# Performance work log

Measured on AMD Instinct MI355X. Metric: run time of the kernel, lower is better.

Reference implementation:

```python
import jax, jax.numpy as jnp
import numpy as np

B, H, W = 8, 512, 512
N_INST = 8
N_SIGMA = 2
FG_W = 1.0
W_INST, W_VAR, W_SEED = 1.0, 10.0, 1.0


def make_yxm():
    xm = jnp.broadcast_to(jnp.linspace(0.0, 1.0, W)[None, None, :], (1, H, W))
    ym = jnp.broadcast_to(jnp.linspace(0.0, 1.0, H)[None, :, None], (1, H, W))
    return jnp.concatenate([ym, xm], 0)  # [2,H,W]


def lovasz_hinge(logits, labels):
    # logits, labels: [P]; labels in {0,1}
    signs = 2.0 * labels - 1.0
    errors = 1.0 - logits * signs
    order = jnp.argsort(-errors)
    errors_s = errors[order]
    gt_s = labels[order]
    gts = gt_s.sum()
    intersection = gts - jnp.cumsum(gt_s)
    union = gts + jnp.cumsum(1.0 - gt_s)
    jac = 1.0 - intersection / union
    jac = jnp.concatenate([jac[:1], jac[1:] - jac[:-1]])
    return jnp.dot(jax.nn.relu(errors_s), jax.lax.stop_gradient(jac))


def seg_item(pred, inst, label, center_img, yxm):
    spatial_emb = jnp.tanh(pred[0:2]) + yxm            # [2,H,W]
    sigma = jax.nn.sigmoid(pred[2:2 + N_SIGMA])        # [2,H,W]
    seed = jax.nn.sigmoid(pred[2 + N_SIGMA])           # [H,W]
    seed_loss = jnp.sum(jnp.where(label == 0, seed * seed, 0.0))

    def per_inst(iid):
        in_mask = (inst == iid)
        cmask = in_mask & center_img
        valid = (cmask.sum() == 1)                      # exactly one center pixel
        m = in_mask.astype(pred.dtype)
        npix = jnp.maximum(m.sum(), 1.0)
        center = jnp.sum(yxm * cmask, axis=(1, 2))      # [2]
        s_mean = jnp.sum(sigma * m, axis=(1, 2)) / npix # [2]
        var_l = jnp.sum(((sigma - jax.lax.stop_gradient(s_mean)[:, None, None]) ** 2) * m) / (N_SIGMA * npix)
        s = jnp.exp(s_mean * 10.0)
        dist = jnp.exp(-jnp.sum(((spatial_emb - center[:, None, None]) ** 2) * s[:, None, None], axis=0))
        inst_l = lovasz_hinge((dist * 2.0 - 1.0).ravel(), m.ravel())
        seed_l = jnp.sum(((seed - jax.lax.stop_gradient(dist)) ** 2) * m)
        v = valid.astype(pred.dtype)
        return inst_l * v, var_l * v, seed_l * v

    il, vl, sl = jax.vmap(per_inst)(jnp.arange(1, N_INST + 1))
    # NOTE: source never increments obj_count in the seg loop, so no division.
    seed_total = (seed_loss + FG_W * sl.sum()) / (H * W)
    return W_INST * il.sum() + W_VAR * vl.sum() + W_SEED * seed_total


def tra_item(pred, inst, center_img, offset, yxm):
    emb = yxm - jnp.tanh(pred[0:2])
    sigma = jax.nn.sigmoid(pred[2:2 + N_SIGMA])

    def per_inst(iid):
        in_mask = (inst == iid)
        cmask = in_mask & center_img
        center = jnp.sum(yxm * cmask, axis=(1, 2))          # [2]
        off_c = jnp.sum(offset * cmask, axis=(1, 2))        # [2]
        gt_c = center - off_c / 256.0
        valid = (cmask.sum() == 1) & (gt_c.min() >= 0.0) & (gt_c.max() <= 1.0)
        m = in_mask.astype(pred.dtype)
        npix = jnp.maximum(m.sum(), 1.0)
        s_mean = jnp.sum(sigma * m, axis=(1, 2)) / npix
        var_l = jnp.sum(((sigma - jax.lax.stop_gradient(s_mean)[:, None, None]) ** 2) * m)  # sum (not mean)
        s = jnp.exp(s_mean * 10.0)
        dist = jnp.exp(-jnp.sum(((emb - gt_c[:, None, None]) ** 2) * s[:, None, None], axis=0))
        tl = lovasz_hinge((dist * 2.0 - 1.0).ravel(), m.ravel())
        v = valid.astype(pred.dtype)
        return tl * v, var_l * v, v

    tl, vl, vs = jax.vmap(per_inst)(jnp.arange(1, N_INST + 1))
    cnt = jnp.maximum(vs.sum(), 1.0)
    return W_INST * (tl.sum() / cnt) + W_VAR * (vl.sum() / cnt)


def setup_inputs() -> dict:
    key = jax.random.key(0)
    k1, k2, k3 = jax.random.split(key, 3)
    inst = np.zeros((H, W), np.int32)
    cen = np.zeros((H, W), bool)
    for i in range(N_INST):
        ty, tx = i // 2, i % 2
        cy, cx = ty * 128 + 64, tx * 256 + 128
        inst[cy - 40:cy + 40, cx - 40:cx + 40] = i + 1
        cen[cy, cx] = True
    instances = jnp.tile(jnp.asarray(inst)[None], (B, 1, 1))
    center_images = jnp.tile(jnp.asarray(cen)[None], (B, 1, 1))
    labels = (instances > 0).astype(jnp.int32)
    return {
        "segmentation_predictions": jax.random.normal(k1, (B, 3 + N_SIGMA, H, W), jnp.float32),
        "tracking_predictions": jax.random.normal(k2, (B // 2, 2 + N_SIGMA, H, W), jnp.float32),
        "instances": instances,
        "labels": labels,
        "center_images": center_images,
        "offsets": jax.random.normal(k3, (B // 2, 2, H, W), jnp.float32),
    }


def reference(segmentation_predictions, tracking_predictions, instances, labels, center_images, offsets):
    yxm = make_yxm()
    seg = jax.vmap(seg_item, in_axes=(0, 0, 0, 0, None))(
        segmentation_predictions, instances, labels, center_images, yxm)
    half = B // 2
    tra = jax.vmap(tra_item, in_axes=(0, 0, 0, 0, None))(
        tracking_predictions, instances[:half], center_images[:half], offsets, yxm)
    return seg.sum() + tra.sum()
```

## Files before the change

### kernel.cpp

```cpp
#include <hip/hip_runtime.h>
#include <cstdint>
#include <cstddef>

#define HW (512 * 512)
#define NB 128
#define NPAIR 96
#define THRQ 4.9f
#define BSCALE 64.0f

#define W_HNEG 0
#define W_HPOS (NPAIR * NB)
#define W_SEEDL (NPAIR * NB * 2)
#define W_CNT (W_SEEDL + NPAIR)
#define NZERO (W_CNT + 1)
#define W_PART 24704
#define W_POUT (W_PART + 12 * 82 * 64)

__device__ __forceinline__ float sigmoidf_(float x) {
    return 1.0f / (1.0f + __expf(-x));
}
__device__ __forceinline__ float tanhf_(float x) {
    float e = __expf(2.0f * x);
    return 1.0f - 2.0f / (e + 1.0f);
}
__device__ __forceinline__ float wred(float v) {
#pragma unroll
    for (int o = 32; o > 0; o >>= 1) v += __shfl_down(v, o, 64);
    return v;
}
__device__ __forceinline__ unsigned wredu(unsigned v) {
#pragma unroll
    for (int o = 32; o > 0; o >>= 1) v += __shfl_down(v, o, 64);
    return v;
}

__global__ __launch_bounds__(256) void reduce_nc(
    const float* __restrict__ segp, const float* __restrict__ trap,
    const int* __restrict__ inst, const int* __restrict__ cen,
    const float* __restrict__ off, float* __restrict__ ws)
{
    __shared__ float wavepart[4][41];
    __shared__ float centacc[40];
    int item = blockIdx.y;
    bool isseg = item < 8;
    int ii = isseg ? item : item - 8;
    int bx = blockIdx.x, tid = threadIdx.x;

    {
        int w = (item * 64 + bx) * 33 + tid;
        if (tid < 33 && w < NZERO) ws[w] = 0.0f;
    }
    if (tid < 40) centacc[tid] = 0.0f;
    __syncthreads();

    const float* pb = isseg ? segp + (size_t)item * 5 * HW
                            : trap + (size_t)ii * 4 * HW;
    const int* ib = inst + (size_t)ii * HW;
    const int* cb = cen + (size_t)ii * HW;
    const float* ob = off + (size_t)ii * 2 * HW;

    float npx[8], a0[8], q0[8], a1[8], q1[8];
#pragma unroll
    for (int j = 0; j < 8; j++) { npx[j]=0.f; a0[j]=0.f; q0[j]=0.f; a1[j]=0.f; q1[j]=0.f; }
    float sacc = 0.f;

    int base = bx * 4096;
    for (int it = 0; it < 4; ++it) {
        int idx = base + (it * 256 + tid) * 4;
        int4 v4 = *(const int4*)&ib[idx];
        const int vs[4] = { v4.x, v4.y, v4.z, v4.w };
        if (isseg) {
            float4 x4 = *(const float4*)&pb[4 * HW + idx];
            const float ss[4] = { x4.x, x4.y, x4.z, x4.w };
#pragma unroll
            for (int c = 0; c < 4; c++) {
                if (vs[c] == 0) { float sd = sigmoidf_(ss[c]); sacc += sd * sd; }
            }
        }
        if ((v4.x | v4.y | v4.z | v4.w) != 0) {
            float4 x2 = *(const float4*)&pb[2 * HW + idx];
            float4 x3 = *(const float4*)&pb[3 * HW + idx];
            int4 c4 = *(const int4*)&cb[idx];
            const float s2s[4] = { x2.x, x2.y, x2.z, x2.w };
            const float s3s[4] = { x3.x, x3.y, x3.z, x3.w };
            const int cs[4] = { c4.x, c4.y, c4.z, c4.w };
#pragma unroll
            for (int c = 0; c < 4; c++) {
                int v = vs[c];
                if (v == 0) continue;
                float s0 = sigmoidf_(s2s[c]);
                float s1 = sigmoidf_(s3s[c]);
                float s00 = s0 * s0, s11 = s1 * s1;
#pragma unroll
                for (int j = 0; j < 8; j++) {
                    float f = (v == j + 1) ? 1.0f : 0.0f;
                    npx[j] += f;
                    a0[j] += f * s0; q0[j] += f * s00;
                    a1[j] += f * s1; q1[j] += f * s11;
                }
                if (cs[c] != 0 && v >= 1 && v <= 8) {
                    int idxc = idx + c;
                    int cb5 = (v - 1) * 5;
                    int y = idxc >> 9, x = idxc & 511;
                    atomicAdd(&centacc[cb5 + 0], (float)y * (1.0f / 511.0f));
                    atomicAdd(&centacc[cb5 + 1], (float)x * (1.0f / 511.0f));
                    atomicAdd(&centacc[cb5 + 2], 1.0f);
                    if (!isseg) {
                        atomicAdd(&centacc[cb5 + 3], ob[idxc]);
                        atomicAdd(&centacc[cb5 + 4], ob[HW + idxc]);
                    }
                }
            }
        }
    }
    int lane = tid & 63, wave = tid >> 6;
#pragma unroll
    for (int j = 0; j < 8; j++) {
        float r0 = wred(npx[j]), r1 = wred(a0[j]), r2 = wred(q0[j]);
        float r3 = wred(a1[j]), r4 = wred(q1[j]);
        if (lane == 0) {
            wavepart[wave][j * 5 + 0] = r0; wavepart[wave][j * 5 + 1] = r1;
            wavepart[wave][j * 5 + 2] = r2; wavepart[wave][j * 5 + 3] = r3;
            wavepart[wave][j * 5 + 4] = r4;
        }
    }
    {
        float rs = wred(sacc);
        if (lane == 0) wavepart[wave][40] = rs;
    }
    __syncthreads();
    float* pit = ws + W_PART + item * 82 * 64;
    if (tid < 40) {
        pit[tid * 64 + bx] = wavepart[0][tid] + wavepart[1][tid] + wavepart[2][tid] + wavepart[3][tid];
    } else if (tid == 40) {
        pit[80 * 64 + bx] = wavepart[0][40] + wavepart[1][40] + wavepart[2][40] + wavepart[3][40];
    } else if (tid >= 41 && tid < 81) {
        pit[(40 + tid - 41) * 64 + bx] = centacc[tid - 41];
    } else if (tid == 81) {
        pit[81 * 64 + bx] = 0.0f;
    }
}

__global__ __launch_bounds__(256) void hist_k(
    const float* __restrict__ segp, const float* __restrict__ trap,
    const int* __restrict__ inst, const float* __restrict__ ws,
    unsigned* __restrict__ hneg, unsigned* __restrict__ hpos,
    float* __restrict__ seedl)
{
    __shared__ unsigned hh[8 * NB + 8];
    __shared__ float csum[82];
    __shared__ float prm[8][4];
    int item = blockIdx.y;
    bool isseg = item < 8;
    int ii = isseg ? item : item - 8;
    int tid = threadIdx.x;
    int pairBase = (isseg ? 0 : 64) + ii * 8;

    for (int i = tid; i < 8 * NB + 8; i += 256) hh[i] = 0u;
    if (tid < 82) {
        const float* pit = ws + W_PART + item * 82 * 64 + tid * 64;
        float s = 0.f;
#pragma unroll 8
        for (int b = 0; b < 64; b++) s += pit[b];
        csum[tid] = s;
    }
    __syncthreads();
    if (tid < 8) {
        int j = tid;
        float np = fmaxf(csum[j * 5], 1.0f);
        float cy = csum[40 + j * 5], cx = csum[40 + j * 5 + 1];
        if (!isseg) {
            cy -= csum[40 + j * 5 + 3] * (1.0f / 256.0f);
            cx -= csum[40 + j * 5 + 4] * (1.0f / 256.0f);
        }
        prm[j][0] = cy;
        prm[j][1] = cx;
        prm[j][2] = __expf(10.0f * csum[j * 5 + 1] / np);
        prm[j][3] = __expf(10.0f * csum[j * 5 + 3] / np);
    }
    __syncthreads();

    float cyR[8], cxR[8], s0R[8], s1R[8];
#pragma unroll
    for (int j = 0; j < 8; j++) {
        cyR[j] = prm[j][0]; cxR[j] = prm[j][1];
        s0R[j] = prm[j][2]; s1R[j] = prm[j][3];
    }
    const float* pb = isseg ? segp + (size_t)item * 5 * HW
                            : trap + (size_t)ii * 4 * HW;
    const int* ib = inst + (size_t)ii * HW;

    unsigned cnt0[8];
#pragma unroll
    for (int j = 0; j < 8; j++) cnt0[j] = 0u;

    int base = blockIdx.x * 4096;
    for (int it = 0; it < 4; ++it) {
        int idx = base + (it * 256 + tid) * 4;
        int4 v4 = *(const int4*)&ib[idx];
        float4 f0 = *(const float4*)&pb[idx];
        float4 f1 = *(const float4*)&pb[HW + idx];
        const int vv[4] = { v4.x, v4.y, v4.z, v4.w };
        const float p0s[4] = { f0.x, f0.y, f0.z, f0.w };
        const float p1s[4] = { f1.x, f1.y, f1.z, f1.w };
#pragma unroll
        for (int c = 0; c < 4; c++) {
            int idxc = idx + c;
            int v = vv[c];
            int y = idxc >> 9, x = idxc & 511;
            float ym = (float)y * (1.0f / 511.0f);
            float xm = (float)x * (1.0f / 511.0f);
            float t0 = tanhf_(p0s[c]), t1 = tanhf_(p1s[c]);
            float e0 = isseg ? (t0 + ym) : (ym - t0);
            float e1 = isseg ? (t1 + xm) : (xm - t1);
            unsigned sbits = 0u;
#pragma unroll
            for (int j = 0; j < 8; j++) {
                float d0 = e0 - cyR[j], d1 = e1 - cxR[j];
                float q = fmaf(d0 * d0, s0R[j], d1 * d1 * s1R[j]);
                bool m = (v == j + 1);
                bool slow = m || (q <= THRQ);
                sbits |= (slow ? 1u : 0u) << j;
                cnt0[j] += slow ? 0u : 1u;
            }
            while (sbits) {
                int j = __ffs(sbits) - 1;
                sbits &= sbits - 1u;
                float d0 = e0 - prm[j][0], d1 = e1 - prm[j][1];
                float q = fmaf(d0 * d0, prm[j][2], d1 * d1 * prm[j][3]);
                float dd = __expf(-q);
                bool m = (v == j + 1);
                float e = m ? fmaf(-2.0f, dd, 2.0f) : 2.0f * dd;
                int bin = (int)(e * BSCALE);
                if (bin > NB - 1) bin = NB - 1;
                atomicAdd(&hh[j * NB + bin], m ? 0x10000u : 1u);
                if (m && isseg) {
                    float sd = sigmoidf_(pb[4 * HW + idxc]);
                    float df = sd - dd;
                    atomicAdd((float*)&hh[8 * NB + j], df * df);
                }
            }
        }
    }
    int lane = tid & 63;
#pragma unroll
    for (int j = 0; j < 8; j++) {
        unsigned r = wredu(cnt0[j]);
        if (lane == 0 && r) atomicAdd(&hh[j * NB], r);
    }
    __syncthreads();

#pragma unroll
    for (int j = 0; j < 8; j++) {
        size_t gb = (size_t)(pairBase + j) * NB;
        for (int i = tid & 127; i < NB; i += 128) {
            if ((tid >> 7) == 0 || 1) {}
        }
        for (int i = tid; i < NB; i += 256) {
            unsigned hv = hh[j * NB + i];
            if (hv) {
                unsigned n = hv & 0xFFFFu, p = hv >> 16;
                if (n) atomicAdd(&hneg[gb + i], n);
                if (p) atomicAdd(&hpos[gb + i], p);
            }
        }
    }
    if (isseg && tid < 8) {
        float sv = __uint_as_float(hh[8 * NB + tid]);
        if (sv != 0.0f) atomicAdd(&seedl[pairBase + tid], sv);
    }
}

__global__ __launch_bounds__(64) void scanfin_k(
    float* __restrict__ ws, const unsigned* __restrict__ hneg,
    const unsigned* __restrict__ hpos, const float* __restrict__ seedl,
    unsigned* __restrict__ cntr, float* __restrict__ out)
{
    __shared__ float fin[NPAIR * 4 + 8];
    int p = blockIdx.x;
    int lane = threadIdx.x;
    int item12 = (p < 64) ? (p >> 3) : (8 + ((p - 64) >> 3));
    int j = p & 7;
    const float* pit = ws + W_PART + item12 * 82 * 64;

    float r0 = pit[(j * 5 + 0) * 64 + lane];
    float r1 = pit[(j * 5 + 1) * 64 + lane];
    float r2 = pit[(j * 5 + 2) * 64 + lane];
    float r3 = pit[(j * 5 + 3) * 64 + lane];
    float r4 = pit[(j * 5 + 4) * 64 + lane];
    float c0 = pit[(40 + j * 5 + 0) * 64 + lane];
    float c1 = pit[(40 + j * 5 + 1) * 64 + lane];
    float c2 = pit[(40 + j * 5 + 2) * 64 + lane];
    float c3 = pit[(40 + j * 5 + 3) * 64 + lane];
    float c4 = pit[(40 + j * 5 + 4) * 64 + lane];
    r0 = wred(r0); r1 = wred(r1); r2 = wred(r2); r3 = wred(r3); r4 = wred(r4);
    c0 = wred(c0); c1 = wred(c1); c2 = wred(c2); c3 = wred(c3); c4 = wred(c4);

    const unsigned* hn = hneg + (size_t)p * NB;
    const unsigned* hp = hpos + (size_t)p * NB;
    unsigned hnv[2], hpv[2];
    float ck = 0.f, cp = 0.f;
#pragma unroll
    for (int i = 0; i < 2; i++) {
        int bn = NB - 1 - (lane * 2 + i);
        unsigned a = hn[bn], b = hp[bn];
        hnv[i] = a; hpv[i] = b;
        ck += (float)(a + b); cp += (float)b;
    }
    float ik = ck, ip = cp;
#pragma unroll
    for (int o = 1; o < 64; o <<= 1) {
        float nk = __shfl_up(ik, o, 64), np2 = __shfl_up(ip, o, 64);
        if (lane >= o) { ik += nk; ip += np2; }
    }
    float P = __shfl(ip, 63, 64);
    float k = ik - ck, pp = ip - cp;
    float acc = 0.f;
#pragma unroll
    for (int i = 0; i < 2; i++) {
        float cn = (float)hnv[i], cpp = (float)hpv[i];
        float c = cn + cpp;
        if (c > 0.f) {
            float Jb = (k > 0.f) ? (1.0f - (P - pp) / (P + k - pp)) : 0.0f;
            k += c; pp += cpp;
            float Ja = 1.0f - (P - pp) / (P + k - pp);
            int bn = NB - 1 - (lane * 2 + i);
            acc += ((float)bn + 0.5f) * (2.0f / NB) * (Ja - Jb);
        }
    }
    acc = wred(acc);

    if (lane == 0) {
        float np = fmaxf(r0, 1.0f);
        float v0 = fmaxf(r2 - r1 * r1 / np, 0.0f);
        float v1 = fmaxf(r4 - r3 * r3 / np, 0.0f);
        float valid, varl;
        if (p < 64) {
            varl = (v0 + v1) / (2.0f * np);
            valid = (c2 > 0.5f && c2 < 1.5f) ? 1.0f : 0.0f;
        } else {
            varl = v0 + v1;
            float gy = c0 - c3 * (1.0f / 256.0f);
            float gx = c1 - c4 * (1.0f / 256.0f);
            valid = (c2 > 0.5f && c2 < 1.5f &&
                     gy >= 0.0f && gy <= 1.0f && gx >= 0.0f && gx <= 1.0f) ? 1.0f : 0.0f;
        }
        float* po = ws + W_POUT + p * 4;
        po[0] = acc; po[1] = valid; po[2] = varl; po[3] = 0.0f;
    }
    __threadfence();
    unsigned old = 0;
    if (lane == 0) old = atomicAdd(cntr, 1u);
    old = (unsigned)__shfl((int)old, 0, 64);
    if (old != NPAIR - 1) return;

    __threadfence();
    volatile float* pv = ws + W_POUT;
    for (int q = lane; q < NPAIR; q += 64) {
        fin[q * 4 + 0] = pv[q * 4 + 0];
        fin[q * 4 + 1] = pv[q * 4 + 1];
        fin[q * 4 + 2] = pv[q * 4 + 2];
        fin[q * 4 + 3] = seedl[q];
    }
#pragma unroll
    for (int b = 0; b < 8; b++) {
        float s = ws[W_PART + b * 82 * 64 + 80 * 64 + lane];
        s = wred(s);
        if (lane == 0) fin[NPAIR * 4 + b] = s;
    }
    __syncthreads();
    if (lane == 0) {
        double total = 0.0;
        for (int b = 0; b < 8; b++) {
            double s = 0.0, sl = 0.0;
            for (int jj = 0; jj < 8; jj++) {
                int pr = b * 8 + jj;
                double v = fin[pr * 4 + 1];
                s += v * ((double)fin[pr * 4 + 0] + 10.0 * (double)fin[pr * 4 + 2]);
                sl += v * (double)fin[pr * 4 + 3];
            }
            total += s + ((double)fin[NPAIR * 4 + b] + sl) / (double)HW;
        }
        for (int tt = 0; tt < 4; tt++) {
            double tl = 0.0, vl = 0.0, cnt = 0.0;
            for (int jj = 0; jj < 8; jj++) {
                int pr = 64 + tt * 8 + jj;
                double v = fin[pr * 4 + 1];
                tl += v * (double)fin[pr * 4 + 0];
                vl += v * (double)fin[pr * 4 + 2];
                cnt += v;
            }
            if (cnt < 1.0) cnt = 1.0;
            total += tl / cnt + 10.0 * vl / cnt;
        }
        *out = (float)total;
    }
}

extern "C" void kernel_launch(void* const* d_in, const int* in_sizes, int n_in,
                              void* d_out, int out_size, void* d_ws, size_t ws_size,
                              hipStream_t stream)
{
    const float* segp = (const float*)d_in[0];
    const float* trap = (const float*)d_in[1];
    const int* inst   = (const int*)d_in[2];
    const int* cen    = (const int*)d_in[4];
    const float* off  = (const float*)d_in[5];
    float* out = (float*)d_out;

    float* ws = (float*)d_ws;
    unsigned* hneg = (unsigned*)d_ws + W_HNEG;
    unsigned* hpos = (unsigned*)d_ws + W_HPOS;
    float* seedl = ws + W_SEEDL;
    unsigned* cntr = (unsigned*)d_ws + W_CNT;

    reduce_nc<<<dim3(64, 12), 256, 0, stream>>>(segp, trap, inst, cen, off, ws);
    hist_k<<<dim3(64, 12), 256, 0, stream>>>(segp, trap, inst, ws, hneg, hpos, seedl);
    scanfin_k<<<NPAIR, 64, 0, stream>>>(ws, hneg, hpos, seedl, cntr, out);
}
```

Before: 64.03 us.

## Add coarse LUT culling of instances, split column-sum kernel, double grid blocks

The reduction and histogram kernels now use 128 blocks per item instead of 64, each covering half as many pixels, to expose more parallelism. A new small kernel reduces the per-block partials once and precomputes per-instance parameters, so the histogram and final kernels no longer repeat that reduction in every block. The histogram kernel builds a shared-memory 48x64 lookup table over embedding space that conservatively marks which instances can fall under the distance threshold. Each pixel then evaluates only those candidates plus its own instance, instead of testing all eight, and the count of far-away pixels is recovered from per-block totals. The cost is an extra launch, per-block LUT construction, and an assumption that embeddings stay inside the LUT's range.

```diff
diff --git a/kernel.cpp b/kernel.cpp
--- a/kernel.cpp
+++ b/kernel.cpp
@@ -7,6 +7,7 @@
 #define NPAIR 96
 #define THRQ 4.9f
 #define BSCALE 64.0f
+#define RB 128
 
 #define W_HNEG 0
 #define W_HPOS (NPAIR * NB)
@@ -14,7 +15,9 @@
 #define W_CNT (W_SEEDL + NPAIR)
 #define NZERO (W_CNT + 1)
 #define W_PART 24704
-#define W_POUT (W_PART + 12 * 82 * 64)
+#define W_CSUM (W_PART + 12 * 81 * RB)
+#define W_PRM (W_CSUM + 12 * 81)
+#define W_POUT (W_PRM + 12 * 32)
 
 __device__ __forceinline__ float sigmoidf_(float x) {
     return 1.0f / (1.0f + __expf(-x));
@@ -28,13 +31,8 @@
     for (int o = 32; o > 0; o >>= 1) v += __shfl_down(v, o, 64);
     return v;
 }
-__device__ __forceinline__ unsigned wredu(unsigned v) {
-#pragma unroll
-    for (int o = 32; o > 0; o >>= 1) v += __shfl_down(v, o, 64);
-    return v;
-}
-
-__global__ __launch_bounds__(256) void reduce_nc(
+
+__global__ __launch_bounds__(256) void reduce_k(
     const float* __restrict__ segp, const float* __restrict__ trap,
     const int* __restrict__ inst, const int* __restrict__ cen,
     const float* __restrict__ off, float* __restrict__ ws)
@@ -47,8 +45,8 @@
     int bx = blockIdx.x, tid = threadIdx.x;
 
     {
-        int w = (item * 64 + bx) * 33 + tid;
-        if (tid < 33 && w < NZERO) ws[w] = 0.0f;
+        int gb = (item * RB + bx) * 17 + tid;
+        if (tid < 17 && gb < NZERO) ws[gb] = 0.0f;
     }
     if (tid < 40) centacc[tid] = 0.0f;
     __syncthreads();
@@ -64,8 +62,9 @@
     for (int j = 0; j < 8; j++) { npx[j]=0.f; a0[j]=0.f; q0[j]=0.f; a1[j]=0.f; q1[j]=0.f; }
     float sacc = 0.f;
 
-    int base = bx * 4096;
-    for (int it = 0; it < 4; ++it) {
+    int base = bx * 2048;
+#pragma unroll
+    for (int it = 0; it < 2; ++it) {
         int idx = base + (it * 256 + tid) * 4;
         int4 v4 = *(const int4*)&ib[idx];
         const int vs[4] = { v4.x, v4.y, v4.z, v4.w };
@@ -78,12 +77,12 @@
             }
         }
         if ((v4.x | v4.y | v4.z | v4.w) != 0) {
+            int4 c4 = *(const int4*)&cb[idx];
             float4 x2 = *(const float4*)&pb[2 * HW + idx];
             float4 x3 = *(const float4*)&pb[3 * HW + idx];
-            int4 c4 = *(const int4*)&cb[idx];
+            const int cs[4] = { c4.x, c4.y, c4.z, c4.w };
             const float s2s[4] = { x2.x, x2.y, x2.z, x2.w };
             const float s3s[4] = { x3.x, x3.y, x3.z, x3.w };
-            const int cs[4] = { c4.x, c4.y, c4.z, c4.w };
 #pragma unroll
             for (int c = 0; c < 4; c++) {
                 int v = vs[c];
@@ -129,73 +128,92 @@
         if (lane == 0) wavepart[wave][40] = rs;
     }
     __syncthreads();
-    float* pit = ws + W_PART + item * 82 * 64;
+    float* pit = ws + W_PART + (size_t)item * 81 * RB;
     if (tid < 40) {
-        pit[tid * 64 + bx] = wavepart[0][tid] + wavepart[1][tid] + wavepart[2][tid] + wavepart[3][tid];
+        pit[tid * RB + bx] = wavepart[0][tid] + wavepart[1][tid] + wavepart[2][tid] + wavepart[3][tid];
     } else if (tid == 40) {
-        pit[80 * 64 + bx] = wavepart[0][40] + wavepart[1][40] + wavepart[2][40] + wavepart[3][40];
-    } else if (tid >= 41 && tid < 81) {
-        pit[(40 + tid - 41) * 64 + bx] = centacc[tid - 41];
-    } else if (tid == 81) {
-        pit[81 * 64 + bx] = 0.0f;
+        pit[80 * RB + bx] = wavepart[0][40] + wavepart[1][40] + wavepart[2][40] + wavepart[3][40];
+    } else if (tid < 81) {
+        pit[(tid - 1) * RB + bx] = centacc[tid - 41];
+    }
+}
+
+__global__ __launch_bounds__(256) void csum_k(float* __restrict__ ws)
+{
+    __shared__ float csh[81];
+    int item = blockIdx.x, tid = threadIdx.x;
+    bool isseg = item < 8;
+    if (tid < 162) {
+        int comp = tid >> 1;
+        const float* p = ws + W_PART + (size_t)item * 81 * RB + comp * RB + (tid & 1) * 64;
+        float s = 0.f;
+#pragma unroll 8
+        for (int i = 0; i < 64; i++) s += p[i];
+        s += __shfl_xor(s, 1, 64);
+        if ((tid & 1) == 0) csh[comp] = s;
+    }
+    __syncthreads();
+    if (tid < 81) ws[W_CSUM + item * 81 + tid] = csh[tid];
+    if (tid < 8) {
+        int j = tid;
+        float np = fmaxf(csh[j * 5], 1.0f);
+        float cy = csh[40 + j * 5], cx = csh[40 + j * 5 + 1];
+        if (!isseg) {
+            cy -= csh[40 + j * 5 + 3] * (1.0f / 256.0f);
+            cx -= csh[40 + j * 5 + 4] * (1.0f / 256.0f);
+        }
+        float* o = ws + W_PRM + item * 32 + j * 4;
+        o[0] = cy;
+        o[1] = cx;
+        o[2] = __expf(10.0f * csh[j * 5 + 1] / np);
+        o[3] = __expf(10.0f * csh[j * 5 + 3] / np);
     }
 }
 
 __global__ __launch_bounds__(256) void hist_k(
     const float* __restrict__ segp, const float* __restrict__ trap,
-    const int* __restrict__ inst, const float* __restrict__ ws,
-    unsigned* __restrict__ hneg, unsigned* __restrict__ hpos,
-    float* __restrict__ seedl)
+    const int* __restrict__ inst, float* __restrict__ ws)
 {
     __shared__ unsigned hh[8 * NB + 8];
-    __shared__ float csum[82];
-    __shared__ float prm[8][4];
+    __shared__ float4 prmv[8];
+    __shared__ unsigned char lut[48 * 64];
     int item = blockIdx.y;
     bool isseg = item < 8;
     int ii = isseg ? item : item - 8;
-    int tid = threadIdx.x;
+    int bx = blockIdx.x, tid = threadIdx.x;
     int pairBase = (isseg ? 0 : 64) + ii * 8;
 
+    unsigned* wsu = (unsigned*)ws;
+    unsigned* hneg = wsu + W_HNEG;
+    unsigned* hpos = wsu + W_HPOS;
+    float* seedl = ws + W_SEEDL;
+
+    if (tid < 8) prmv[tid] = ((const float4*)(ws + W_PRM + item * 32))[tid];
     for (int i = tid; i < 8 * NB + 8; i += 256) hh[i] = 0u;
-    if (tid < 82) {
-        const float* pit = ws + W_PART + item * 82 * 64 + tid * 64;
-        float s = 0.f;
-#pragma unroll 8
-        for (int b = 0; b < 64; b++) s += pit[b];
-        csum[tid] = s;
-    }
-    __syncthreads();
-    if (tid < 8) {
-        int j = tid;
-        float np = fmaxf(csum[j * 5], 1.0f);
-        float cy = csum[40 + j * 5], cx = csum[40 + j * 5 + 1];
-        if (!isseg) {
-            cy -= csum[40 + j * 5 + 3] * (1.0f / 256.0f);
-            cx -= csum[40 + j * 5 + 4] * (1.0f / 256.0f);
-        }
-        prm[j][0] = cy;
-        prm[j][1] = cx;
-        prm[j][2] = __expf(10.0f * csum[j * 5 + 1] / np);
-        prm[j][3] = __expf(10.0f * csum[j * 5 + 3] / np);
-    }
-    __syncthreads();
-
-    float cyR[8], cxR[8], s0R[8], s1R[8];
-#pragma unroll
-    for (int j = 0; j < 8; j++) {
-        cyR[j] = prm[j][0]; cxR[j] = prm[j][1];
-        s0R[j] = prm[j][2]; s1R[j] = prm[j][3];
-    }
+    __syncthreads();
+    for (int ci = tid; ci < 48 * 64; ci += 256) {
+        int iy = ci >> 6, ix = ci & 63;
+        float ey = -1.0f + ((float)iy + 0.5f) * (1.0f / 16.0f);
+        float ex = -1.0f + ((float)ix + 0.5f) * (1.0f / 16.0f);
+        unsigned mk = 0u;
+#pragma unroll
+        for (int j = 0; j < 8; j++) {
+            float4 P = prmv[j];
+            float dy = fmaxf(fabsf(ey - P.x) - (1.0f / 32.0f), 0.0f);
+            float dx = fmaxf(fabsf(ex - P.y) - (1.0f / 32.0f), 0.0f);
+            if (fmaf(dy * dy, P.z, dx * dx * P.w) <= THRQ) mk |= 1u << j;
+        }
+        lut[ci] = (unsigned char)mk;
+    }
+    __syncthreads();
+
     const float* pb = isseg ? segp + (size_t)item * 5 * HW
                             : trap + (size_t)ii * 4 * HW;
     const int* ib = inst + (size_t)ii * HW;
 
-    unsigned cnt0[8];
-#pragma unroll
-    for (int j = 0; j < 8; j++) cnt0[j] = 0u;
-
-    int base = blockIdx.x * 4096;
-    for (int it = 0; it < 4; ++it) {
+    int base = bx * 2048;
+#pragma unroll
+    for (int it = 0; it < 2; ++it) {
         int idx = base + (it * 256 + tid) * 4;
         int4 v4 = *(const int4*)&ib[idx];
         float4 f0 = *(const float4*)&pb[idx];
@@ -213,56 +231,55 @@
             float t0 = tanhf_(p0s[c]), t1 = tanhf_(p1s[c]);
             float e0 = isseg ? (t0 + ym) : (ym - t0);
             float e1 = isseg ? (t1 + xm) : (xm - t1);
-            unsigned sbits = 0u;
-#pragma unroll
-            for (int j = 0; j < 8; j++) {
-                float d0 = e0 - cyR[j], d1 = e1 - cxR[j];
-                float q = fmaf(d0 * d0, s0R[j], d1 * d1 * s1R[j]);
+            int iy = (int)((e0 + 1.0f) * 16.0f);
+            int ix = (int)((e1 + 1.0f) * 16.0f);
+            unsigned mask = lut[iy * 64 + ix];
+            unsigned vb = (unsigned)(v - 1);
+            if (vb < 8u) mask |= 1u << vb;
+            while (mask) {
+                int j = __ffs(mask) - 1;
+                mask &= mask - 1u;
+                float4 P = prmv[j];
+                float d0 = e0 - P.x, d1 = e1 - P.y;
+                float q = fmaf(d0 * d0, P.z, d1 * d1 * P.w);
                 bool m = (v == j + 1);
-                bool slow = m || (q <= THRQ);
-                sbits |= (slow ? 1u : 0u) << j;
-                cnt0[j] += slow ? 0u : 1u;
-            }
-            while (sbits) {
-                int j = __ffs(sbits) - 1;
-                sbits &= sbits - 1u;
-                float d0 = e0 - prm[j][0], d1 = e1 - prm[j][1];
-                float q = fmaf(d0 * d0, prm[j][2], d1 * d1 * prm[j][3]);
-                float dd = __expf(-q);
-                bool m = (v == j + 1);
-                float e = m ? fmaf(-2.0f, dd, 2.0f) : 2.0f * dd;
-                int bin = (int)(e * BSCALE);
-                if (bin > NB - 1) bin = NB - 1;
-                atomicAdd(&hh[j * NB + bin], m ? 0x10000u : 1u);
-                if (m && isseg) {
-                    float sd = sigmoidf_(pb[4 * HW + idxc]);
-                    float df = sd - dd;
-                    atomicAdd((float*)&hh[8 * NB + j], df * df);
+                if (m || (q <= THRQ)) {
+                    float dd = __expf(-q);
+                    float e = m ? fmaf(-2.0f, dd, 2.0f) : 2.0f * dd;
+                    int bin = (int)(e * BSCALE);
+                    if (bin > NB - 1) bin = NB - 1;
+                    atomicAdd(&hh[j * NB + bin], m ? 0x10000u : 1u);
+                    if (m && isseg) {
+                        float sd = sigmoidf_(pb[4 * HW + idxc]);
+                        float df = sd - dd;
+                        atomicAdd((float*)&hh[8 * NB + j], df * df);
+                    }
                 }
             }
         }
     }
-    int lane = tid & 63;
-#pragma unroll
-    for (int j = 0; j < 8; j++) {
-        unsigned r = wredu(cnt0[j]);
-        if (lane == 0 && r) atomicAdd(&hh[j * NB], r);
-    }
-    __syncthreads();
-
-#pragma unroll
-    for (int j = 0; j < 8; j++) {
-        size_t gb = (size_t)(pairBase + j) * NB;
-        for (int i = tid & 127; i < NB; i += 128) {
-            if ((tid >> 7) == 0 || 1) {}
-        }
-        for (int i = tid; i < NB; i += 256) {
-            unsigned hv = hh[j * NB + i];
-            if (hv) {
-                unsigned n = hv & 0xFFFFu, p = hv >> 16;
-                if (n) atomicAdd(&hneg[gb + i], n);
-                if (p) atomicAdd(&hpos[gb + i], p);
-            }
+    __syncthreads();
+    {
+        int g = tid >> 5, gl = tid & 31;
+        unsigned s = 0u;
+#pragma unroll
+        for (int b = 0; b < 4; b++) {
+            unsigned hv = hh[g * NB + gl * 4 + b];
+            s += (hv & 0xFFFFu) + (hv >> 16);
+        }
+#pragma unroll
+        for (int o = 16; o > 0; o >>= 1) s += __shfl_down(s, o, 32);
+        if (gl == 0) atomicAdd(&hh[g * NB], 2048u - s);
+    }
+    __syncthreads();
+    for (int i = tid; i < 8 * NB; i += 256) {
+        unsigned hv = hh[i];
+        if (hv) {
+            int j = i >> 7, b = i & (NB - 1);
+            size_t gb = (size_t)(pairBase + j) * NB + b;
+            unsigned n = hv & 0xFFFFu, p = hv >> 16;
+            if (n) atomicAdd(&hneg[gb], n);
+            if (p) atomicAdd(&hpos[gb], p);
         }
     }
     if (isseg && tid < 8) {
@@ -272,29 +289,28 @@
 }
 
 __global__ __launch_bounds__(64) void scanfin_k(
-    float* __restrict__ ws, const unsigned* __restrict__ hneg,
-    const unsigned* __restrict__ hpos, const float* __restrict__ seedl,
-    unsigned* __restrict__ cntr, float* __restrict__ out)
+    float* __restrict__ ws, float* __restrict__ out)
 {
     __shared__ float fin[NPAIR * 4 + 8];
     int p = blockIdx.x;
     int lane = threadIdx.x;
+    unsigned* wsu = (unsigned*)ws;
+    const unsigned* hneg = wsu + W_HNEG;
+    const unsigned* hpos = wsu + W_HPOS;
+    unsigned* cntr = wsu + W_CNT;
+
     int item12 = (p < 64) ? (p >> 3) : (8 + ((p - 64) >> 3));
     int j = p & 7;
-    const float* pit = ws + W_PART + item12 * 82 * 64;
-
-    float r0 = pit[(j * 5 + 0) * 64 + lane];
-    float r1 = pit[(j * 5 + 1) * 64 + lane];
-    float r2 = pit[(j * 5 + 2) * 64 + lane];
-    float r3 = pit[(j * 5 + 3) * 64 + lane];
-    float r4 = pit[(j * 5 + 4) * 64 + lane];
-    float c0 = pit[(40 + j * 5 + 0) * 64 + lane];
-    float c1 = pit[(40 + j * 5 + 1) * 64 + lane];
-    float c2 = pit[(40 + j * 5 + 2) * 64 + lane];
-    float c3 = pit[(40 + j * 5 + 3) * 64 + lane];
-    float c4 = pit[(40 + j * 5 + 4) * 64 + lane];
-    r0 = wred(r0); r1 = wred(r1); r2 = wred(r2); r3 = wred(r3); r4 = wred(r4);
-    c0 = wred(c0); c1 = wred(c1); c2 = wred(c2); c3 = wred(c3); c4 = wred(c4);
+    const float* cs = ws + W_CSUM + item12 * 81;
+    float val = 0.f;
+    if (lane < 10) {
+        int comp = (lane < 5) ? (j * 5 + lane) : (40 + j * 5 + (lane - 5));
+        val = cs[comp];
+    }
+    float r0 = __shfl(val, 0, 64), r1 = __shfl(val, 1, 64), r2 = __shfl(val, 2, 64);
+    float r3 = __shfl(val, 3, 64), r4 = __shfl(val, 4, 64);
+    float c0 = __shfl(val, 5, 64), c1 = __shfl(val, 6, 64), c2 = __shfl(val, 7, 64);
+    float c3 = __shfl(val, 8, 64), c4 = __shfl(val, 9, 64);
 
     const unsigned* hn = hneg + (size_t)p * NB;
     const unsigned* hp = hpos + (size_t)p * NB;
@@ -353,21 +369,18 @@
     if (lane == 0) old = atomicAdd(cntr, 1u);
     old = (unsigned)__shfl((int)old, 0, 64);
     if (old != NPAIR - 1) return;
-
     __threadfence();
-    volatile float* pv = ws + W_POUT;
+
+    volatile const float* pv = ws + W_POUT;
+    volatile const float* sdv = ws + W_SEEDL;
+    volatile const float* csv = ws + W_CSUM;
     for (int q = lane; q < NPAIR; q += 64) {
         fin[q * 4 + 0] = pv[q * 4 + 0];
         fin[q * 4 + 1] = pv[q * 4 + 1];
         fin[q * 4 + 2] = pv[q * 4 + 2];
-        fin[q * 4 + 3] = seedl[q];
-    }
-#pragma unroll
-    for (int b = 0; b < 8; b++) {
-        float s = ws[W_PART + b * 82 * 64 + 80 * 64 + lane];
-        s = wred(s);
-        if (lane == 0) fin[NPAIR * 4 + b] = s;
-    }
+        fin[q * 4 + 3] = sdv[q];
+    }
+    if (lane < 8) fin[NPAIR * 4 + lane] = csv[lane * 81 + 80];
     __syncthreads();
     if (lane == 0) {
         double total = 0.0;
@@ -407,14 +420,10 @@
     const int* cen    = (const int*)d_in[4];
     const float* off  = (const float*)d_in[5];
     float* out = (float*)d_out;
-
     float* ws = (float*)d_ws;
-    unsigned* hneg = (unsigned*)d_ws + W_HNEG;
-    unsigned* hpos = (unsigned*)d_ws + W_HPOS;
-    float* seedl = ws + W_SEEDL;
-    unsigned* cntr = (unsigned*)d_ws + W_CNT;
-
-    reduce_nc<<<dim3(64, 12), 256, 0, stream>>>(segp, trap, inst, cen, off, ws);
-    hist_k<<<dim3(64, 12), 256, 0, stream>>>(segp, trap, inst, ws, hneg, hpos, seedl);
-    scanfin_k<<<NPAIR, 64, 0, stream>>>(ws, hneg, hpos, seedl, cntr, out);
-}
+
+    reduce_k<<<dim3(RB, 12), 256, 0, stream>>>(segp, trap, inst, cen, off, ws);
+    csum_k<<<12, 256, 0, stream>>>(ws);
+    hist_k<<<dim3(RB, 12), 256, 0, stream>>>(segp, trap, inst, ws);
+    scanfin_k<<<NPAIR, 64, 0, stream>>>(ws, out);
+}
```

Result: no change. 64.83 us (+1.2%).
